# Kernel optimization log

Hardware: AMD Instinct MI355X
Metric: run time of the kernel (lower is better)

Reference implementation:

```python
import jax, jax.numpy as jnp
import numpy as np

G_ZERO_INIT = 32.0  # g initialized to log2(g0^2 - g0)


def setup_inputs() -> dict:
    key = jax.random.key(0)
    k1, k2, k3 = jax.random.split(key, 3)
    B, L, D = 64, 16384, 64
    query = jax.random.normal(k1, (B, 1, D), dtype=jnp.float32)
    keys = jax.random.normal(k2, (B, L, D), dtype=jnp.float32)
    values = jax.random.normal(k3, (B, L, 1), dtype=jnp.float32)
    g = jnp.asarray(np.log2(G_ZERO_INIT**2 - G_ZERO_INIT), dtype=jnp.float32)
    return {"query": query, "keys": keys, "values": values, "g": g, "k": 256}


def reference(query, keys, values, g, k):
    # cosine similarity between query (B,1,D) and keys (B,L,D) -> (B,L)
    qn = query / jnp.linalg.norm(query, axis=-1, keepdims=True)
    kn = keys / jnp.linalg.norm(keys, axis=-1, keepdims=True)
    similarity = jnp.einsum("bqd,bld->bl", qn, kn) * g  # (B, L)
    # top-k select + batched gather of values
    top_sim, idx = jax.lax.top_k(similarity, k)          # (B, k) each
    values_sel = jnp.take_along_axis(values, idx[:, :, None], axis=1)  # (B, k, 1)
    weights = jax.nn.softmax(top_sim, axis=-1)           # (B, k)
    return values_sel, weights
```

## Files before the change

### kernel.cpp

```cpp
#include <hip/hip_runtime.h>
#include <math.h>

#define BATCH 64
#define LSEQ  16384
#define DIM   64
#define KSEL  256

__global__ __launch_bounds__(256) void sim_kernel(
    const float* __restrict__ q,
    const float* __restrict__ keys,
    const float* __restrict__ gp,
    double* __restrict__ sims)
{
    const int b     = blockIdx.x >> 6;
    const int chunk = blockIdx.x & 63;
    const int t  = threadIdx.x;
    const int j  = t & 15;
    const int rl = t >> 4;

    const float4* q4 = reinterpret_cast<const float4*>(q) + b * 16;
    float4 qv = q4[j];
    const double qx = qv.x, qy = qv.y, qz = qv.z, qw = qv.w;
    double qss = qx*qx + qy*qy + qz*qz + qw*qw;
    #pragma unroll
    for (int m = 1; m < 16; m <<= 1) qss += __shfl_xor(qss, m);
    const double scale = (double)gp[0] / sqrt(qss);

    __shared__ double local[256];
    const float4* k4 = reinterpret_cast<const float4*>(keys) + (size_t)b * LSEQ * 16;
    const int row_base = chunk * 256;

    for (int it = 0; it < 16; ++it) {
        const int row = row_base + it * 16 + rl;
        float4 kv = k4[row * 16 + j];
        const double kx = kv.x, ky = kv.y, kz = kv.z, kw = kv.w;
        double dot = qx*kx + qy*ky + qz*kz + qw*kw;
        double kss = kx*kx + ky*ky + kz*kz + kw*kw;
        #pragma unroll
        for (int m = 1; m < 16; m <<= 1) {
            dot += __shfl_xor(dot, m);
            kss += __shfl_xor(kss, m);
        }
        if (j == 0) local[it * 16 + rl] = scale * dot / sqrt(kss);
    }
    __syncthreads();
    sims[(size_t)b * LSEQ + row_base + t] = local[t];
}

__global__ __launch_bounds__(256, 1) void topk_kernel(
    const double* __restrict__ sims,
    const float* __restrict__ values,
    float* __restrict__ out)
{
    const int b = blockIdx.x;
    const int t = threadIdx.x;
    const double* s = sims + (size_t)b * LSEQ;

    unsigned long long skey[64];
    #pragma unroll
    for (int it = 0; it < 64; ++it) {
        unsigned long long u =
            (unsigned long long)__double_as_longlong(s[it * 256 + t]);
        skey[it] = (u >> 63) ? ~u : (u | 0x8000000000000000ull);
    }

    __shared__ unsigned hist[256];
    __shared__ unsigned scan[256];
    __shared__ ulonglong2 cand[512];
    __shared__ unsigned sh_prefix, sh_mask, sh_k, ccount;

    if (t == 0) { sh_prefix = 0u; sh_mask = 0u; sh_k = KSEL; ccount = 0u; }

    for (int p = 0; p < 4; ++p) {
        const int shift = 24 - 8 * p;
        hist[t] = 0u;
        __syncthreads();
        const unsigned prefix = sh_prefix;
        const unsigned mask   = sh_mask;
        const unsigned kcur   = sh_k;
        #pragma unroll
        for (int it = 0; it < 64; ++it) {
            unsigned hi = (unsigned)(skey[it] >> 32);
            if (((hi ^ prefix) & mask) == 0u)
                atomicAdd(&hist[(hi >> shift) & 255u], 1u);
        }
        __syncthreads();
        scan[t] = hist[t];
        __syncthreads();
        #pragma unroll
        for (int off = 1; off < 256; off <<= 1) {
            unsigned v = (t + off < 256) ? scan[t + off] : 0u;
            __syncthreads();
            scan[t] += v;
            __syncthreads();
        }
        if (scan[t] >= kcur && (t == 255 || scan[t + 1] < kcur)) {
            sh_prefix = prefix | ((unsigned)t << shift);
            sh_mask   = mask | (0xFFu << shift);
            sh_k      = kcur - ((t == 255) ? 0u : scan[t + 1]);
        }
        __syncthreads();
    }
    const unsigned T32 = sh_prefix;

    #pragma unroll
    for (int it = 0; it < 64; ++it) {
        unsigned long long key = skey[it];
        if ((unsigned)(key >> 32) >= T32) {
            unsigned pos = atomicAdd(&ccount, 1u);
            if (pos < 512u) {
                unsigned idx = (unsigned)(it * 256 + t);
                cand[pos] = make_ulonglong2(
                    key, (unsigned long long)(0xFFFFFFFFu - idx));
            }
        }
    }
    __syncthreads();
    const unsigned total = ccount < 512u ? ccount : 512u;
    for (int i = t; i < 512; i += 256)
        if ((unsigned)i >= total) cand[i] = make_ulonglong2(0ull, 0ull);

    for (int size = 2; size <= 512; size <<= 1) {
        for (int stride = size >> 1; stride > 0; stride >>= 1) {
            __syncthreads();
            int i  = ((t & ~(stride - 1)) << 1) | (t & (stride - 1));
            int jj = i + stride;
            bool up = ((i & size) == 0);
            ulonglong2 a = cand[i], c = cand[jj];
            bool agt = (a.x > c.x) || (a.x == c.x && a.y > c.y);
            if (agt == up) { cand[i] = c; cand[jj] = a; }
        }
    }
    __syncthreads();

    ulonglong2 v = cand[511 - t];
    unsigned idx = 0xFFFFFFFFu - (unsigned)v.y;
    unsigned long long ub = (v.x & 0x8000000000000000ull)
                          ? (v.x ^ 0x8000000000000000ull) : ~v.x;
    double sv = __longlong_as_double((long long)ub);

    ulonglong2 vm = cand[511];
    unsigned long long um = (vm.x & 0x8000000000000000ull)
                          ? (vm.x ^ 0x8000000000000000ull) : ~vm.x;
    double fm = __longlong_as_double((long long)um);

    double e = exp(sv - fm);
    double esum = e;
    #pragma unroll
    for (int m = 1; m < 64; m <<= 1) esum += __shfl_xor(esum, m);
    __shared__ double wsum[4];
    if ((t & 63) == 0) wsum[t >> 6] = esum;
    __syncthreads();
    const double tot = wsum[0] + wsum[1] + wsum[2] + wsum[3];

    out[b * KSEL + t]                = values[(size_t)b * LSEQ + idx];
    out[BATCH * KSEL + b * KSEL + t] = (float)(e / tot);
}

extern "C" void kernel_launch(void* const* d_in, const int* in_sizes, int n_in,
                              void* d_out, int out_size, void* d_ws, size_t ws_size,
                              hipStream_t stream)
{
    const float* q      = (const float*)d_in[0];
    const float* keys   = (const float*)d_in[1];
    const float* values = (const float*)d_in[2];
    const float* g      = (const float*)d_in[3];
    float* out   = (float*)d_out;
    double* sims = (double*)d_ws;

    sim_kernel<<<dim3(BATCH * (LSEQ / 256)), dim3(256), 0, stream>>>(q, keys, g, sims);
    topk_kernel<<<dim3(BATCH), dim3(256), 0, stream>>>(sims, values, out);
}
```

Measured before the change: 403.7 us.

## Split top-k into per-chunk bitonic sort stage and merge stage

Replaces the single-block-per-batch radix-select top-k with two kernels. The first sorts 2048-element chunks in shared memory across 512 blocks and writes each chunk's top 256 as candidates. The second bitonic-sorts 2048 candidates per batch to pick the final top-k. The aim is to use more CUs than the 64-block radix select did, at the cost of an extra launch, a workspace round trip, and full bitonic sorts that do more work than the radix selection. Stage1 sorts on only the high 32 key bits plus the index, so ties in those bits are ordered by index rather than by the full value, which can pick the wrong candidates within a chunk.

Result: slower. 436.9 us (+8.2%).

```diff
diff --git a/kernel.cpp b/kernel.cpp
--- a/kernel.cpp
+++ b/kernel.cpp
@@ -5,6 +5,9 @@
 #define LSEQ  16384
 #define DIM   64
 #define KSEL  256
+#define CHUNK 2048
+#define NCHUNK (LSEQ / CHUNK)
+#define NCAND (NCHUNK * KSEL)
 
 __global__ __launch_bounds__(256) void sim_kernel(
     const float* __restrict__ q,
@@ -47,102 +50,98 @@
     sims[(size_t)b * LSEQ + row_base + t] = local[t];
 }
 
-__global__ __launch_bounds__(256, 1) void topk_kernel(
+__device__ __forceinline__ unsigned long long f64_sortable(double v) {
+    unsigned long long u = (unsigned long long)__double_as_longlong(v);
+    return (u >> 63) ? ~u : (u | 0x8000000000000000ull);
+}
+__device__ __forceinline__ double sortable_f64(unsigned long long k) {
+    unsigned long long u = (k & 0x8000000000000000ull)
+                         ? (k ^ 0x8000000000000000ull) : ~k;
+    return __longlong_as_double((long long)u);
+}
+
+__global__ __launch_bounds__(256) void stage1_kernel(
     const double* __restrict__ sims,
+    ulonglong2* __restrict__ cand)
+{
+    const int b     = blockIdx.x >> 3;
+    const int chunk = blockIdx.x & 7;
+    const int t     = threadIdx.x;
+    const int base  = chunk * CHUNK;
+    const double* s = sims + (size_t)b * LSEQ + base;
+
+    __shared__ unsigned long long items[CHUNK];
+    __shared__ unsigned lo[CHUNK];
+
+    #pragma unroll
+    for (int it = 0; it < CHUNK / 256; ++it) {
+        int lidx = it * 256 + t;
+        unsigned long long key = f64_sortable(s[lidx]);
+        items[lidx] = (key & 0xFFFFFFFF00000000ull) |
+                      (unsigned long long)(0xFFFFFFFFu - (unsigned)lidx);
+        lo[lidx] = (unsigned)key;
+    }
+
+    for (int size = 2; size <= CHUNK; size <<= 1) {
+        for (int stride = size >> 1; stride > 0; stride >>= 1) {
+            __syncthreads();
+            #pragma unroll
+            for (int r = 0; r < CHUNK / 512; ++r) {
+                int tt = r * 256 + t;
+                int i  = ((tt & ~(stride - 1)) << 1) | (tt & (stride - 1));
+                int jj = i + stride;
+                bool up = ((i & size) == 0);
+                unsigned long long a = items[i], c = items[jj];
+                if ((a > c) == up) { items[i] = c; items[jj] = a; }
+            }
+        }
+    }
+    __syncthreads();
+
+    unsigned long long item = items[CHUNK - 1 - t];
+    unsigned lidx = 0xFFFFFFFFu - (unsigned)item;
+    unsigned long long fullkey = (item & 0xFFFFFFFF00000000ull) |
+                                 (unsigned long long)lo[lidx];
+    cand[((size_t)b * NCHUNK + chunk) * KSEL + t] =
+        make_ulonglong2(fullkey, (unsigned long long)(base + lidx));
+}
+
+__global__ __launch_bounds__(256) void stage2_kernel(
+    const ulonglong2* __restrict__ cand,
     const float* __restrict__ values,
     float* __restrict__ out)
 {
     const int b = blockIdx.x;
     const int t = threadIdx.x;
-    const double* s = sims + (size_t)b * LSEQ;
+    const ulonglong2* c = cand + (size_t)b * NCAND;
 
-    unsigned long long skey[64];
-    #pragma unroll
-    for (int it = 0; it < 64; ++it) {
-        unsigned long long u =
-            (unsigned long long)__double_as_longlong(s[it * 256 + t]);
-        skey[it] = (u >> 63) ? ~u : (u | 0x8000000000000000ull);
-    }
-
-    __shared__ unsigned hist[256];
-    __shared__ unsigned scan[256];
-    __shared__ ulonglong2 cand[512];
-    __shared__ unsigned sh_prefix, sh_mask, sh_k, ccount;
-
-    if (t == 0) { sh_prefix = 0u; sh_mask = 0u; sh_k = KSEL; ccount = 0u; }
-
-    for (int p = 0; p < 4; ++p) {
-        const int shift = 24 - 8 * p;
-        hist[t] = 0u;
-        __syncthreads();
-        const unsigned prefix = sh_prefix;
-        const unsigned mask   = sh_mask;
-        const unsigned kcur   = sh_k;
-        #pragma unroll
-        for (int it = 0; it < 64; ++it) {
-            unsigned hi = (unsigned)(skey[it] >> 32);
-            if (((hi ^ prefix) & mask) == 0u)
-                atomicAdd(&hist[(hi >> shift) & 255u], 1u);
-        }
-        __syncthreads();
-        scan[t] = hist[t];
-        __syncthreads();
-        #pragma unroll
-        for (int off = 1; off < 256; off <<= 1) {
-            unsigned v = (t + off < 256) ? scan[t + off] : 0u;
-            __syncthreads();
-            scan[t] += v;
-            __syncthreads();
-        }
-        if (scan[t] >= kcur && (t == 255 || scan[t + 1] < kcur)) {
-            sh_prefix = prefix | ((unsigned)t << shift);
-            sh_mask   = mask | (0xFFu << shift);
-            sh_k      = kcur - ((t == 255) ? 0u : scan[t + 1]);
-        }
-        __syncthreads();
-    }
-    const unsigned T32 = sh_prefix;
+    __shared__ ulonglong2 arr[NCAND];
 
     #pragma unroll
-    for (int it = 0; it < 64; ++it) {
-        unsigned long long key = skey[it];
-        if ((unsigned)(key >> 32) >= T32) {
-            unsigned pos = atomicAdd(&ccount, 1u);
-            if (pos < 512u) {
-                unsigned idx = (unsigned)(it * 256 + t);
-                cand[pos] = make_ulonglong2(
-                    key, (unsigned long long)(0xFFFFFFFFu - idx));
+    for (int it = 0; it < NCAND / 256; ++it)
+        arr[it * 256 + t] = c[it * 256 + t];
+
+    for (int size = 2; size <= NCAND; size <<= 1) {
+        for (int stride = size >> 1; stride > 0; stride >>= 1) {
+            __syncthreads();
+            #pragma unroll
+            for (int r = 0; r < NCAND / 512; ++r) {
+                int tt = r * 256 + t;
+                int i  = ((tt & ~(stride - 1)) << 1) | (tt & (stride - 1));
+                int jj = i + stride;
+                bool up = ((i & size) == 0);
+                ulonglong2 a = arr[i], cc = arr[jj];
+                bool agt = (a.x > cc.x) || (a.x == cc.x && a.y < cc.y);
+                if (agt == up) { arr[i] = cc; arr[jj] = a; }
             }
         }
     }
     __syncthreads();
-    const unsigned total = ccount < 512u ? ccount : 512u;
-    for (int i = t; i < 512; i += 256)
-        if ((unsigned)i >= total) cand[i] = make_ulonglong2(0ull, 0ull);
 
-    for (int size = 2; size <= 512; size <<= 1) {
-        for (int stride = size >> 1; stride > 0; stride >>= 1) {
-            __syncthreads();
-            int i  = ((t & ~(stride - 1)) << 1) | (t & (stride - 1));
-            int jj = i + stride;
-            bool up = ((i & size) == 0);
-            ulonglong2 a = cand[i], c = cand[jj];
-            bool agt = (a.x > c.x) || (a.x == c.x && a.y > c.y);
-            if (agt == up) { cand[i] = c; cand[jj] = a; }
-        }
-    }
-    __syncthreads();
-
-    ulonglong2 v = cand[511 - t];
-    unsigned idx = 0xFFFFFFFFu - (unsigned)v.y;
-    unsigned long long ub = (v.x & 0x8000000000000000ull)
-                          ? (v.x ^ 0x8000000000000000ull) : ~v.x;
-    double sv = __longlong_as_double((long long)ub);
-
-    ulonglong2 vm = cand[511];
-    unsigned long long um = (vm.x & 0x8000000000000000ull)
-                          ? (vm.x ^ 0x8000000000000000ull) : ~vm.x;
-    double fm = __longlong_as_double((long long)um);
+    ulonglong2 v = arr[NCAND - 1 - t];
+    unsigned idx = (unsigned)v.y;
+    double sv = sortable_f64(v.x);
+    double fm = sortable_f64(arr[NCAND - 1].x);
 
     double e = exp(sv - fm);
     double esum = e;
@@ -166,8 +165,11 @@
     const float* values = (const float*)d_in[2];
     const float* g      = (const float*)d_in[3];
     float* out   = (float*)d_out;
-    double* sims = (double*)d_ws;
+
+    double* sims     = (double*)d_ws;
+    ulonglong2* cand = (ulonglong2*)((char*)d_ws + (size_t)BATCH * LSEQ * 8);
 
     sim_kernel<<<dim3(BATCH * (LSEQ / 256)), dim3(256), 0, stream>>>(q, keys, g, sims);
-    topk_kernel<<<dim3(BATCH), dim3(256), 0, stream>>>(sims, values, out);
+    stage1_kernel<<<dim3(BATCH * NCHUNK), dim3(256), 0, stream>>>(sims, cand);
+    stage2_kernel<<<dim3(BATCH), dim3(256), 0, stream>>>(cand, values, out);
 }
```
